# Optimization experiments

Hardware: AMD Instinct MI355X
Metric: run time of the kernel (lower is better)

## Reference

```python
import jax, jax.numpy as jnp
import numpy as np


def setup_inputs() -> dict:
    key = jax.random.key(0)
    ks = jax.random.split(key, 5)
    B, S, D_in, D_out, E, R = 4, 1024, 1024, 1024, 8, 16
    x = jax.random.normal(ks[0], (B, S, D_in), dtype=jnp.float32)
    weight = jax.random.normal(ks[1], (D_out, D_in), dtype=jnp.float32) / np.sqrt(D_in)
    gate_w = jax.random.normal(ks[2], (E, D_in), dtype=jnp.float32) / np.sqrt(D_in)
    lora_U = jax.random.normal(ks[3], (E, R, D_in), dtype=jnp.float32) / np.sqrt(D_in)
    lora_V = jax.random.normal(ks[4], (E, D_out, R), dtype=jnp.float32) / np.sqrt(R)
    return {"x": x, "weight": weight, "gate_w": gate_w, "lora_U": lora_U, "lora_V": lora_V}


def reference(x, weight, gate_w, lora_U, lora_V):
    # MoELoRA forward (global_gating=False), lora_alpha=1.0, rank=16
    scaling = 1.0 / lora_U.shape[1]
    B, S, D_in = x.shape
    xt = x.reshape(-1, D_in)                      # (N, D_in), N = B*S
    # per-token softmax gate over experts
    gate = jax.nn.softmax(xt @ gate_w.T, axis=-1)  # (N, E)
    # base term: sum_e gate[n,e] * (W @ x_n) = W @ x_n since gate sums to 1
    base = xt @ weight.T                           # (N, D_out)
    # low-rank expert contributions without materializing (E, D_out, D_in)
    t = jnp.einsum('nh,erh->ner', xt, lora_U)      # (N, E, R)
    lora = jnp.einsum('ne,eor,ner->no', gate, lora_V, t)  # (N, D_out)
    out = base + scaling * lora
    return out.reshape(B, S, -1)
```

## Files before the change

kernel.cpp:

```cpp
#include <hip/hip_runtime.h>
#include <hip/hip_bf16.h>

typedef __attribute__((ext_vector_type(8))) short short8;
typedef __attribute__((ext_vector_type(4))) float f32x4;

#define NTOK 4096
#define DIN  1024
#define DOUT 1024
#define KTOT 1152
#define XLD  1152
#define TLDS 200

__device__ __forceinline__ unsigned short f2bf(float f) {
    __hip_bfloat16 h = __float2bfloat16(f);
    return __builtin_bit_cast(unsigned short, h);
}

__device__ __forceinline__ void gload16(const void* g, void* l) {
    __builtin_amdgcn_global_load_lds((const __attribute__((address_space(1))) void*)g,
                                     (__attribute__((address_space(3))) void*)l, 16, 0, 0);
}

__device__ __forceinline__ uint4 pack8(const float* s) {
    float4 v0 = *(const float4*)s, v1 = *(const float4*)(s + 4);
    union { unsigned short u[8]; uint4 q; } pk;
    pk.u[0] = f2bf(v0.x); pk.u[1] = f2bf(v0.y); pk.u[2] = f2bf(v0.z); pk.u[3] = f2bf(v0.w);
    pk.u[4] = f2bf(v1.x); pk.u[5] = f2bf(v1.y); pk.u[6] = f2bf(v1.z); pk.u[7] = f2bf(v1.w);
    return pk.q;
}

__global__ __launch_bounds__(256) void k_cvtuw(const float* __restrict__ lora_U,
                                               const float* __restrict__ gate_w,
                                               const float* __restrict__ w,
                                               const float* __restrict__ lora_V,
                                               __hip_bfloat16* __restrict__ Ucat,
                                               __hip_bfloat16* __restrict__ Wcat) {
    int b = blockIdx.x;
    if (b < 96) {
        int idx = b * 256 + threadIdx.x;
        int r = idx >> 7, g = idx & 127;
        uint4 q = make_uint4(0u, 0u, 0u, 0u);
        if (r < 128)      q = pack8(lora_U + (size_t)r * DIN + g * 8);
        else if (r < 136) q = pack8(gate_w + (size_t)(r - 128) * DIN + g * 8);
        *(uint4*)(Ucat + (size_t)r * DIN + g * 8) = q;
    } else {
        int idx = (b - 96) * 256 + threadIdx.x;
        int o = idx / 144, g = idx - o * 144;
        const float* s;
        if (g < 128) s = w + (size_t)o * DIN + g * 8;
        else {
            int i0 = (g - 128) * 8;
            int e = i0 >> 4, r = i0 & 15;
            s = lora_V + (size_t)e * (DOUT * 16) + (size_t)o * 16 + r;
        }
        *(uint4*)(Wcat + (size_t)o * KTOT + g * 8) = pack8(s);
    }
}

__global__ __launch_bounds__(256) void k_gemm1f(const float* __restrict__ x,
                                                const __hip_bfloat16* __restrict__ Ucat,
                                                __hip_bfloat16* __restrict__ Xcat) {
    __shared__ char smem[28672];
    __hip_bfloat16* Asm = (__hip_bfloat16*)smem;
    __hip_bfloat16* Bsm = (__hip_bfloat16*)(smem + 2048);
    float (*Tsm)[TLDS] = (float(*)[TLDS])smem;

    const int t = threadIdx.x, lane = t & 63, wid = t >> 6;
    const int row0 = blockIdx.x * 16;
    const int l7 = lane & 7, l8 = lane >> 3, l15 = lane & 15, l16 = lane >> 4;
    const int scol = ((l7 ^ l8) << 3);

    f32x4 acc[3];
#pragma unroll
    for (int n = 0; n < 3; ++n) acc[n] = (f32x4){0.f, 0.f, 0.f, 0.f};

    const int ar = (t & 127) >> 3;
    const int ac8 = (t & 7) * 8;
    const int abyte = ar * 128 + (((t & 7) ^ (ar & 7)) << 4);

    int boff[3];
#pragma unroll
    for (int n = 0; n < 3; ++n) boff[n] = (wid * 48 + n * 16 + l15) * 128;
    const int aoff = l15 * 128;
    int sw[2];
#pragma unroll
    for (int ks = 0; ks < 2; ++ks) sw[ks] = (((ks * 4 + l16) ^ l7) << 4);

    for (int kt = 0; kt < 16; ++kt) {
        const int k0 = kt << 6;
        if (t < 128) {
            uint4 q = pack8(x + (size_t)(row0 + ar) * DIN + k0 + ac8);
            *(uint4*)((char*)Asm + abyte) = q;
            *(uint4*)(Xcat + (size_t)(row0 + ar) * XLD + k0 + ac8) = q;
        }
#pragma unroll
        for (int i = 0; i < 6; ++i) {
            int cj = wid * 6 + i;
            gload16(Ucat + (size_t)(cj * 8 + l8) * DIN + k0 + scol,
                    (char*)Bsm + cj * 1024);
        }
        __syncthreads();
#pragma unroll
        for (int ks = 0; ks < 2; ++ks) {
            short8 af = *(const short8*)((const char*)Asm + aoff + sw[ks]);
#pragma unroll
            for (int n = 0; n < 3; ++n) {
                short8 bf = *(const short8*)((const char*)Bsm + boff[n] + sw[ks]);
                acc[n] = __builtin_amdgcn_mfma_f32_16x16x32_bf16(af, bf, acc[n], 0, 0, 0);
            }
        }
        __syncthreads();
    }

#pragma unroll
    for (int n = 0; n < 3; ++n)
#pragma unroll
        for (int j = 0; j < 4; ++j)
            Tsm[l16 * 4 + j][wid * 48 + n * 16 + l15] = acc[n][j];
    __syncthreads();

    if (t < 128) {
        const int tok = t >> 3, e = t & 7;
        float l[8];
#pragma unroll
        for (int i = 0; i < 8; ++i) l[i] = Tsm[tok][128 + i];
        float m = l[0];
#pragma unroll
        for (int i = 1; i < 8; ++i) m = fmaxf(m, l[i]);
        float s = 0.f;
#pragma unroll
        for (int i = 0; i < 8; ++i) s += __expf(l[i] - m);
        const float g = __expf(l[e] - m) / s * 0.0625f;
        union { unsigned short u[16]; uint4 q[2]; } pk;
#pragma unroll
        for (int jj = 0; jj < 16; ++jj) pk.u[jj] = f2bf(g * Tsm[tok][e * 16 + jj]);
        uint4* dst = (uint4*)(Xcat + (size_t)(row0 + tok) * XLD + 1024 + e * 16);
        dst[0] = pk.q[0]; dst[1] = pk.q[1];
    }
}

__global__ __launch_bounds__(256) void k_gemm2(const __hip_bfloat16* __restrict__ A,
                                               const __hip_bfloat16* __restrict__ B,
                                               float* __restrict__ out) {
    __shared__ __hip_bfloat16 Asm[64 * 64];
    __shared__ __hip_bfloat16 Bsm[64 * 64];
    const int b = blockIdx.x;
    const int xcd = b & 7, j = b >> 3;
    const int bx = xcd * 8 + (j & 7), by = j >> 3;
    const int row0 = bx * 64, col0 = by * 64;

    const int t = threadIdx.x, lane = t & 63, wid = t >> 6;
    const int wr = wid >> 1, wc = wid & 1;
    const int l7 = lane & 7, l8 = lane >> 3, l15 = lane & 15, l16 = lane >> 4;
    const int scol = ((l7 ^ l8) << 3);

    f32x4 zf = {0.f, 0.f, 0.f, 0.f};
    f32x4 acc[2][2];
#pragma unroll
    for (int m = 0; m < 2; ++m)
#pragma unroll
        for (int n = 0; n < 2; ++n) acc[m][n] = zf;

    int aoff[2], boff[2], sw[2];
#pragma unroll
    for (int m = 0; m < 2; ++m) aoff[m] = (wr * 32 + m * 16 + l15) * 128;
#pragma unroll
    for (int n = 0; n < 2; ++n) boff[n] = (wc * 32 + n * 16 + l15) * 128;
#pragma unroll
    for (int ks = 0; ks < 2; ++ks) sw[ks] = (((ks * 4 + l16) ^ l7) << 4);

    for (int kt = 0; kt < 18; ++kt) {
        const int k0 = kt << 6;
#pragma unroll
        for (int i = 0; i < 2; ++i) {
            int ci = wid * 2 + i;
            gload16(A + (size_t)(row0 + ci * 8 + l8) * XLD + k0 + scol,
                    (char*)Asm + ci * 1024);
            gload16(B + (size_t)(col0 + ci * 8 + l8) * KTOT + k0 + scol,
                    (char*)Bsm + ci * 1024);
        }
        __syncthreads();
#pragma unroll
        for (int ks = 0; ks < 2; ++ks) {
            short8 af[2], bf[2];
#pragma unroll
            for (int m = 0; m < 2; ++m)
                af[m] = *(const short8*)((const char*)Asm + aoff[m] + sw[ks]);
#pragma unroll
            for (int n = 0; n < 2; ++n)
                bf[n] = *(const short8*)((const char*)Bsm + boff[n] + sw[ks]);
#pragma unroll
            for (int m = 0; m < 2; ++m)
#pragma unroll
                for (int n = 0; n < 2; ++n)
                    acc[m][n] = __builtin_amdgcn_mfma_f32_16x16x32_bf16(af[m], bf[n], acc[m][n], 0, 0, 0);
        }
        __syncthreads();
    }

#pragma unroll
    for (int m = 0; m < 2; ++m)
#pragma unroll
        for (int n = 0; n < 2; ++n)
#pragma unroll
            for (int jj = 0; jj < 4; ++jj)
                out[(size_t)(row0 + wr * 32 + m * 16 + l16 * 4 + jj) * DOUT
                    + col0 + wc * 32 + n * 16 + l15] = acc[m][n][jj];
}

extern "C" void kernel_launch(void* const* d_in, const int* in_sizes, int n_in,
                              void* d_out, int out_size, void* d_ws, size_t ws_size,
                              hipStream_t stream) {
    const float* x      = (const float*)d_in[0];
    const float* weight = (const float*)d_in[1];
    const float* gate_w = (const float*)d_in[2];
    const float* lora_U = (const float*)d_in[3];
    const float* lora_V = (const float*)d_in[4];
    float* out = (float*)d_out;

    char* ws = (char*)d_ws;
    __hip_bfloat16* Xcat = (__hip_bfloat16*)ws;
    __hip_bfloat16* Ucat = (__hip_bfloat16*)(ws + 9437184);
    __hip_bfloat16* Wcat = (__hip_bfloat16*)(ws + 9437184 + 393216);

    k_cvtuw<<<672, 256, 0, stream>>>(lora_U, gate_w, weight, lora_V, Ucat, Wcat);
    k_gemm1f<<<256, 256, 0, stream>>>(x, Ucat, Xcat);
    k_gemm2<<<1024, 256, 0, stream>>>(Xcat, Wcat, out);
}
```

Baseline: 43.74 us.

## Double-buffer LDS in both GEMM kernels and enlarge gemm2 tile to 128x64

Result: faster. 41.13 us (-6.0%).

```diff
diff --git a/kernel.cpp b/kernel.cpp
--- a/kernel.cpp
+++ b/kernel.cpp
@@ -21,12 +21,15 @@
                                      (__attribute__((address_space(3))) void*)l, 16, 0, 0);
 }
 
-__device__ __forceinline__ uint4 pack8(const float* s) {
-    float4 v0 = *(const float4*)s, v1 = *(const float4*)(s + 4);
+__device__ __forceinline__ uint4 pack2(float4 v0, float4 v1) {
     union { unsigned short u[8]; uint4 q; } pk;
     pk.u[0] = f2bf(v0.x); pk.u[1] = f2bf(v0.y); pk.u[2] = f2bf(v0.z); pk.u[3] = f2bf(v0.w);
     pk.u[4] = f2bf(v1.x); pk.u[5] = f2bf(v1.y); pk.u[6] = f2bf(v1.z); pk.u[7] = f2bf(v1.w);
     return pk.q;
+}
+
+__device__ __forceinline__ uint4 pack8(const float* s) {
+    return pack2(*(const float4*)s, *(const float4*)(s + 4));
 }
 
 __global__ __launch_bounds__(256) void k_cvtuw(const float* __restrict__ lora_U,
@@ -60,9 +63,7 @@
 __global__ __launch_bounds__(256) void k_gemm1f(const float* __restrict__ x,
                                                 const __hip_bfloat16* __restrict__ Ucat,
                                                 __hip_bfloat16* __restrict__ Xcat) {
-    __shared__ char smem[28672];
-    __hip_bfloat16* Asm = (__hip_bfloat16*)smem;
-    __hip_bfloat16* Bsm = (__hip_bfloat16*)(smem + 2048);
+    __shared__ char smem[53248];
     float (*Tsm)[TLDS] = (float(*)[TLDS])smem;
 
     const int t = threadIdx.x, lane = t & 63, wid = t >> 6;
@@ -86,30 +87,54 @@
 #pragma unroll
     for (int ks = 0; ks < 2; ++ks) sw[ks] = (((ks * 4 + l16) ^ l7) << 4);
 
+    if (t < 128) {
+        uint4 q = pack8(x + (size_t)(row0 + ar) * DIN + 0 + ac8);
+        *(uint4*)(smem + 0 * 2048 + abyte) = q;
+        *(uint4*)(Xcat + (size_t)(row0 + ar) * XLD + 0 + ac8) = q;
+    }
+#pragma unroll
+    for (int i = 0; i < 6; ++i) {
+        int cj = wid * 6 + i;
+        gload16(Ucat + (size_t)(cj * 8 + l8) * DIN + 0 + scol,
+                smem + 4096 + cj * 1024);
+    }
+    __syncthreads();
+
+    int cur = 0;
     for (int kt = 0; kt < 16; ++kt) {
-        const int k0 = kt << 6;
-        if (t < 128) {
-            uint4 q = pack8(x + (size_t)(row0 + ar) * DIN + k0 + ac8);
-            *(uint4*)((char*)Asm + abyte) = q;
-            *(uint4*)(Xcat + (size_t)(row0 + ar) * XLD + k0 + ac8) = q;
-        }
-#pragma unroll
-        for (int i = 0; i < 6; ++i) {
-            int cj = wid * 6 + i;
-            gload16(Ucat + (size_t)(cj * 8 + l8) * DIN + k0 + scol,
-                    (char*)Bsm + cj * 1024);
-        }
-        __syncthreads();
+        const bool hasNext = kt < 15;
+        const int k1 = (kt + 1) << 6;
+        float4 f0, f1;
+        if (hasNext && t < 128) {
+            const float* s = x + (size_t)(row0 + ar) * DIN + k1 + ac8;
+            f0 = *(const float4*)s; f1 = *(const float4*)(s + 4);
+        }
+        if (hasNext) {
+#pragma unroll
+            for (int i = 0; i < 6; ++i) {
+                int cj = wid * 6 + i;
+                gload16(Ucat + (size_t)(cj * 8 + l8) * DIN + k1 + scol,
+                        smem + 4096 + (cur ^ 1) * 24576 + cj * 1024);
+            }
+        }
+        const char* Ab = smem + cur * 2048;
+        const char* Bb = smem + 4096 + cur * 24576;
 #pragma unroll
         for (int ks = 0; ks < 2; ++ks) {
-            short8 af = *(const short8*)((const char*)Asm + aoff + sw[ks]);
+            short8 af = *(const short8*)(Ab + aoff + sw[ks]);
 #pragma unroll
             for (int n = 0; n < 3; ++n) {
-                short8 bf = *(const short8*)((const char*)Bsm + boff[n] + sw[ks]);
+                short8 bf = *(const short8*)(Bb + boff[n] + sw[ks]);
                 acc[n] = __builtin_amdgcn_mfma_f32_16x16x32_bf16(af, bf, acc[n], 0, 0, 0);
             }
         }
+        if (hasNext && t < 128) {
+            uint4 q = pack2(f0, f1);
+            *(uint4*)(smem + (cur ^ 1) * 2048 + abyte) = q;
+            *(uint4*)(Xcat + (size_t)(row0 + ar) * XLD + k1 + ac8) = q;
+        }
         __syncthreads();
+        cur ^= 1;
     }
 
 #pragma unroll
@@ -142,12 +167,11 @@
 __global__ __launch_bounds__(256) void k_gemm2(const __hip_bfloat16* __restrict__ A,
                                                const __hip_bfloat16* __restrict__ B,
                                                float* __restrict__ out) {
-    __shared__ __hip_bfloat16 Asm[64 * 64];
-    __shared__ __hip_bfloat16 Bsm[64 * 64];
+    __shared__ char smem[49152];
     const int b = blockIdx.x;
     const int xcd = b & 7, j = b >> 3;
-    const int bx = xcd * 8 + (j & 7), by = j >> 3;
-    const int row0 = bx * 64, col0 = by * 64;
+    const int bx = xcd * 4 + (j & 3), by = j >> 2;
+    const int row0 = bx * 128, col0 = by * 64;
 
     const int t = threadIdx.x, lane = t & 63, wid = t >> 6;
     const int wr = wid >> 1, wc = wid & 1;
@@ -155,57 +179,80 @@
     const int scol = ((l7 ^ l8) << 3);
 
     f32x4 zf = {0.f, 0.f, 0.f, 0.f};
-    f32x4 acc[2][2];
-#pragma unroll
-    for (int m = 0; m < 2; ++m)
+    f32x4 acc[4][2];
+#pragma unroll
+    for (int m = 0; m < 4; ++m)
 #pragma unroll
         for (int n = 0; n < 2; ++n) acc[m][n] = zf;
 
-    int aoff[2], boff[2], sw[2];
-#pragma unroll
-    for (int m = 0; m < 2; ++m) aoff[m] = (wr * 32 + m * 16 + l15) * 128;
+    int aoff[4], boff[2], sw[2];
+#pragma unroll
+    for (int m = 0; m < 4; ++m) aoff[m] = (wr * 64 + m * 16 + l15) * 128;
 #pragma unroll
     for (int n = 0; n < 2; ++n) boff[n] = (wc * 32 + n * 16 + l15) * 128;
 #pragma unroll
     for (int ks = 0; ks < 2; ++ks) sw[ks] = (((ks * 4 + l16) ^ l7) << 4);
 
-    for (int kt = 0; kt < 18; ++kt) {
-        const int k0 = kt << 6;
-#pragma unroll
-        for (int i = 0; i < 2; ++i) {
-            int ci = wid * 2 + i;
-            gload16(A + (size_t)(row0 + ci * 8 + l8) * XLD + k0 + scol,
-                    (char*)Asm + ci * 1024);
-            gload16(B + (size_t)(col0 + ci * 8 + l8) * KTOT + k0 + scol,
-                    (char*)Bsm + ci * 1024);
-        }
+#define G2_STAGE(buf, kt)                                                      \
+    {                                                                          \
+        const int k0_ = (kt) << 6;                                             \
+        _Pragma("unroll")                                                      \
+        for (int i = 0; i < 4; ++i) {                                          \
+            int ci = wid * 4 + i;                                              \
+            gload16(A + (size_t)(row0 + ci * 8 + l8) * XLD + k0_ + scol,       \
+                    smem + (buf) * 16384 + ci * 1024);                         \
+        }                                                                      \
+        _Pragma("unroll")                                                      \
+        for (int i = 0; i < 2; ++i) {                                          \
+            int cj = wid * 2 + i;                                              \
+            gload16(B + (size_t)(col0 + cj * 8 + l8) * KTOT + k0_ + scol,      \
+                    smem + 32768 + (buf) * 8192 + cj * 1024);                  \
+        }                                                                      \
+    }
+
+#define G2_COMP(buf)                                                           \
+    {                                                                          \
+        const char* Ab = smem + (buf) * 16384;                                 \
+        const char* Bb = smem + 32768 + (buf) * 8192;                          \
+        _Pragma("unroll")                                                      \
+        for (int ks = 0; ks < 2; ++ks) {                                       \
+            short8 af[4], bf[2];                                               \
+            _Pragma("unroll")                                                  \
+            for (int m = 0; m < 4; ++m)                                        \
+                af[m] = *(const short8*)(Ab + aoff[m] + sw[ks]);               \
+            _Pragma("unroll")                                                  \
+            for (int n = 0; n < 2; ++n)                                        \
+                bf[n] = *(const short8*)(Bb + boff[n] + sw[ks]);               \
+            _Pragma("unroll")                                                  \
+            for (int m = 0; m < 4; ++m)                                        \
+                _Pragma("unroll")                                              \
+                for (int n = 0; n < 2; ++n)                                    \
+                    acc[m][n] = __builtin_amdgcn_mfma_f32_16x16x32_bf16(       \
+                        af[m], bf[n], acc[m][n], 0, 0, 0);                     \
+        }                                                                      \
+    }
+
+    G2_STAGE(0, 0);
+    __syncthreads();
+    int cur = 0;
+    for (int kt = 0; kt < 17; ++kt) {
+        G2_STAGE(cur ^ 1, kt + 1);
+        G2_COMP(cur);
         __syncthreads();
-#pragma unroll
-        for (int ks = 0; ks < 2; ++ks) {
-            short8 af[2], bf[2];
-#pragma unroll
-            for (int m = 0; m < 2; ++m)
-                af[m] = *(const short8*)((const char*)Asm + aoff[m] + sw[ks]);
-#pragma unroll
-            for (int n = 0; n < 2; ++n)
-                bf[n] = *(const short8*)((const char*)Bsm + boff[n] + sw[ks]);
-#pragma unroll
-            for (int m = 0; m < 2; ++m)
-#pragma unroll
-                for (int n = 0; n < 2; ++n)
-                    acc[m][n] = __builtin_amdgcn_mfma_f32_16x16x32_bf16(af[m], bf[n], acc[m][n], 0, 0, 0);
-        }
-        __syncthreads();
-    }
-
-#pragma unroll
-    for (int m = 0; m < 2; ++m)
+        cur ^= 1;
+    }
+    G2_COMP(cur);
+
+#pragma unroll
+    for (int m = 0; m < 4; ++m)
 #pragma unroll
         for (int n = 0; n < 2; ++n)
 #pragma unroll
             for (int jj = 0; jj < 4; ++jj)
-                out[(size_t)(row0 + wr * 32 + m * 16 + l16 * 4 + jj) * DOUT
+                out[(size_t)(row0 + wr * 64 + m * 16 + l16 * 4 + jj) * DOUT
                     + col0 + wc * 32 + n * 16 + l15] = acc[m][n][jj];
+#undef G2_STAGE
+#undef G2_COMP
 }
 
 extern "C" void kernel_launch(void* const* d_in, const int* in_sizes, int n_in,
@@ -225,5 +272,5 @@
 
     k_cvtuw<<<672, 256, 0, stream>>>(lora_U, gate_w, weight, lora_V, Ucat, Wcat);
     k_gemm1f<<<256, 256, 0, stream>>>(x, Ucat, Xcat);
-    k_gemm2<<<1024, 256, 0, stream>>>(Xcat, Wcat, out);
-}
+    k_gemm2<<<512, 256, 0, stream>>>(Xcat, Wcat, out);
+}
```
